# Optimization experiments

Hardware: AMD Instinct MI355X
Metric: run time of the kernel (lower is better)

## Reference

```python
import jax, jax.numpy as jnp
import numpy as np

LEN_M = 131328   # (data_dim+1) * d_h = 513 * 256
D_H = 256
N_MC = 64
DATA_DIM_P1 = 513
N = 4096


def setup_inputs() -> dict:
    key = jax.random.key(0)
    k1, k2, k3, k4 = jax.random.split(key, 4)
    params = jax.random.normal(k1, (2 * LEN_M,), dtype=jnp.float32)
    W1 = jax.random.normal(k2, (D_H + 1,), dtype=jnp.float32)
    x = jax.random.normal(k3, (N, DATA_DIM_P1), dtype=jnp.float32)
    eps = jax.random.normal(k4, (N_MC,), dtype=jnp.float32)
    return {"params": params, "W1": W1, "x": x, "eps": eps}


def reference(params, W1, x, eps):
    # split variational params into means and (relu'd) variances
    m_w0 = params[:LEN_M]                                  # [len_m]
    v_w0 = jax.nn.relu(params[LEN_M:]) + 1e-6              # [len_m]
    # reparameterized MC sampling; NOTE: torch code draws ONE scalar eps per
    # MC sample (randn(m_w0[0].shape) is scalar), shared across all weights.
    samps_w0 = m_w0[:, None] + eps[None, :] * jnp.sqrt(v_w0)[:, None]  # [len_m, M]
    W0 = samps_w0.reshape(DATA_DIM_P1, D_H, N_MC)          # [d+1, h, M]
    # fused batched GEMM replacing the d_h * num_MC_samps tiny matmuls
    x_w0 = jnp.einsum('nd,dhm->nhm', x, W0)                # [N, h, M]
    z = jax.nn.relu(x_w0)
    ones = jnp.ones((x.shape[0], 1, N_MC), dtype=x.dtype)
    z = jnp.concatenate([ones, z], axis=1)                 # [N, h+1, M]
    pred_samps = jnp.einsum('nhm,h->nm', z, W1)            # [N, M]
    return pred_samps, m_w0, v_w0
```

## Files before the change

kernel.cpp:

```cpp
#include <hip/hip_runtime.h>
#include <hip/hip_bf16.h>
#include <math.h>

#define LEN_M   131328
#define D_H     256
#define N_MC    64
#define D_P1    513
#define NROW    4096
#define KPAD    512
#define PRED_ELEMS (NROW * N_MC)

#define XB_ELEMS   (NROW * KPAD)
#define WCBT_ELEMS (512 * 512)

typedef __attribute__((ext_vector_type(8))) short short8;
typedef __attribute__((ext_vector_type(4))) float floatx4;

__global__ __launch_bounds__(256) void prep_kernel(
    const float* __restrict__ params, const float* __restrict__ x,
    float* __restrict__ out, __hip_bfloat16* __restrict__ xb,
    float* __restrict__ wcl, __hip_bfloat16* __restrict__ wcbt)
{
    __shared__ unsigned short T[64][65];
    const int bid = blockIdx.x;
    const int t   = threadIdx.x;

    if (bid < 8192) {
        int i = bid * 256 + t;
        int row = i >> 9, col = i & 511;
        xb[i] = __float2bfloat16(x[row * D_P1 + col]);
        if (i < PRED_ELEMS) out[i] = 0.0f;
        if (i < LEN_M) {
            float m = params[i];
            float v = fmaxf(params[LEN_M + i], 0.0f) + 1e-6f;
            out[PRED_ELEMS + i]         = m;
            out[PRED_ELEMS + LEN_M + i] = v;
            if (i >= 131072) {
                int h = i - 131072;
                wcl[h]       = m;
                wcl[256 + h] = sqrtf(v);
            }
        }
        return;
    }

    const int b2 = bid - 8192;
    const int k0 = (b2 & 7) * 64;
    const int c0 = (b2 >> 3) * 64;
    const int hh = t & 63, kb = t >> 6;
    const bool spart = (c0 >= 256);
    const int hbase = c0 & 255;
    const float* src = params + (spart ? LEN_M : 0);

    #pragma unroll 4
    for (int p = 0; p < 16; ++p) {
        int kk = p * 4 + kb;
        float v = src[(k0 + kk) * 256 + hbase + hh];
        if (spart) v = sqrtf(fmaxf(v, 0.0f) + 1e-6f);
        __hip_bfloat16 b = __float2bfloat16(v);
        T[kk][hh] = *(unsigned short*)&b;
    }
    __syncthreads();

    const int cc = t >> 2, kq = t & 3;
    short8 lo, hi;
    #pragma unroll
    for (int j = 0; j < 8; ++j) lo[j] = (short)T[kq * 16 + j][cc];
    #pragma unroll
    for (int j = 0; j < 8; ++j) hi[j] = (short)T[kq * 16 + 8 + j][cc];
    short* dst = (short*)wcbt + (c0 + cc) * 512 + k0 + kq * 16;
    *(short8*)dst       = lo;
    *(short8*)(dst + 8) = hi;
}

__global__ __launch_bounds__(256) void main_kernel(
    const __hip_bfloat16* __restrict__ xb, const __hip_bfloat16* __restrict__ wcbt,
    const float* __restrict__ wcl, const float* __restrict__ x,
    const float* __restrict__ W1, const float* __restrict__ eps,
    float* __restrict__ out)
{
    __shared__ float Clds[128 * 20];

    const int t = threadIdx.x;
    const int w = t >> 6, lane = t & 63;
    const int lane15 = lane & 15, quad = lane >> 4;
    const int H  = blockIdx.x;
    const int bm = blockIdx.y * 16;

    const int part  = w >> 1;
    const int sub   = (w & 1) * 32;
    const int lcol0 = part * 64 + sub;
    const int gc0   = part * 256 + H * 64 + sub + lane15;

    const float e = eps[lane];
    const int r0 = quad * 4;
    float xl[4];
    #pragma unroll
    for (int r = 0; r < 4; ++r) xl[r] = x[(bm + r0 + r) * D_P1 + 512];

    const short* ap  = (const short*)xb   + (bm + lane15) * 512 + quad * 8;
    const short* bp0 = (const short*)wcbt + (gc0 +  0) * 512 + quad * 8;
    const short* bp1 = (const short*)wcbt + (gc0 + 16) * 512 + quad * 8;

    floatx4 acc0 = {0.f,0.f,0.f,0.f}, acc1 = acc0;

    #pragma unroll 4
    for (int k0 = 0; k0 < 512; k0 += 32) {
        short8 a  = *(const short8*)(ap  + k0);
        short8 b0 = *(const short8*)(bp0 + k0);
        short8 b1 = *(const short8*)(bp1 + k0);
        acc0 = __builtin_amdgcn_mfma_f32_16x16x32_bf16(a, b0, acc0, 0, 0, 0);
        acc1 = __builtin_amdgcn_mfma_f32_16x16x32_bf16(a, b1, acc1, 0, 0, 0);
    }

    floatx4 accs[2] = {acc0, acc1};
    #pragma unroll
    for (int s = 0; s < 2; ++s) {
        const float wl = wcl[gc0 + s * 16];
        float4 vv;
        vv.x = accs[s][0] + xl[0] * wl;
        vv.y = accs[s][1] + xl[1] * wl;
        vv.z = accs[s][2] + xl[2] * wl;
        vv.w = accs[s][3] + xl[3] * wl;
        const int lcol = lcol0 + s * 16 + lane15;
        *(float4*)&Clds[lcol * 20 + r0] = vv;
    }
    __syncthreads();

    const int rb = w * 4;
    const float init = (H == 0) ? W1[0] : 0.0f;
    float accp[4] = {init, init, init, init};

    #pragma unroll 8
    for (int hl = 0; hl < 64; ++hl) {
        const float w1h = W1[1 + H * 64 + hl];
        const float4 a0 = *(const float4*)&Clds[hl * 20 + rb];
        const float4 b0 = *(const float4*)&Clds[(64 + hl) * 20 + rb];
        accp[0] = fmaf(fmaxf(fmaf(e, b0.x, a0.x), 0.f), w1h, accp[0]);
        accp[1] = fmaf(fmaxf(fmaf(e, b0.y, a0.y), 0.f), w1h, accp[1]);
        accp[2] = fmaf(fmaxf(fmaf(e, b0.z, a0.z), 0.f), w1h, accp[2]);
        accp[3] = fmaf(fmaxf(fmaf(e, b0.w, a0.w), 0.f), w1h, accp[3]);
    }

    float* op = out + (bm + rb) * 64 + lane;
    #pragma unroll
    for (int r = 0; r < 4; ++r)
        unsafeAtomicAdd(op + r * 64, accp[r]);
}

extern "C" void kernel_launch(void* const* d_in, const int* in_sizes, int n_in,
                              void* d_out, int out_size, void* d_ws, size_t ws_size,
                              hipStream_t stream)
{
    const float* params = (const float*)d_in[0];
    const float* W1     = (const float*)d_in[1];
    const float* x      = (const float*)d_in[2];
    const float* eps    = (const float*)d_in[3];
    float* out = (float*)d_out;

    __hip_bfloat16* xb   = (__hip_bfloat16*)d_ws;
    __hip_bfloat16* wcbt = xb + XB_ELEMS;
    float*          wcl  = (float*)(wcbt + WCBT_ELEMS);

    prep_kernel<<<8192 + 64, 256, 0, stream>>>(params, x, out, xb, wcl, wcbt);
    main_kernel<<<dim3(4, 256), 256, 0, stream>>>(xb, wcbt, wcl, x, W1, eps, out);
}
```

Before: 99.98 us.

## Stage GEMM tiles in LDS via direct loads and replace atomics with partial-sum reduce

The main kernel now processes 32 rows per block and stages A and B tiles into LDS with global_load_lds, so each loaded tile is shared across waves instead of every wave reading its own operands from global memory. Each wave computes four 16x16 MFMA outputs. The per-H results are written to a partial buffer rather than atomically added to the output, and a new reduce kernel sums the four partials and adds the bias. This also removes the zeroing of the output in the prep kernel. The cost is an extra kernel launch, more partial-buffer memory traffic, and two block-wide barriers per k-step that leave no overlap between loads and compute.

```diff
diff --git a/kernel.cpp b/kernel.cpp
--- a/kernel.cpp
+++ b/kernel.cpp
@@ -16,6 +16,13 @@
 typedef __attribute__((ext_vector_type(8))) short short8;
 typedef __attribute__((ext_vector_type(4))) float floatx4;
 
+__device__ __forceinline__ void gl_lds16(const void* g, void* l)
+{
+    __builtin_amdgcn_global_load_lds(
+        (const __attribute__((address_space(1))) unsigned int*)g,
+        (__attribute__((address_space(3))) unsigned int*)l, 16, 0, 0);
+}
+
 __global__ __launch_bounds__(256) void prep_kernel(
     const float* __restrict__ params, const float* __restrict__ x,
     float* __restrict__ out, __hip_bfloat16* __restrict__ xb,
@@ -29,7 +36,6 @@
         int i = bid * 256 + t;
         int row = i >> 9, col = i & 511;
         xb[i] = __float2bfloat16(x[row * D_P1 + col]);
-        if (i < PRED_ELEMS) out[i] = 0.0f;
         if (i < LEN_M) {
             float m = params[i];
             float v = fmaxf(params[LEN_M + i], 0.0f) + 1e-6f;
@@ -77,75 +83,124 @@
     const __hip_bfloat16* __restrict__ xb, const __hip_bfloat16* __restrict__ wcbt,
     const float* __restrict__ wcl, const float* __restrict__ x,
     const float* __restrict__ W1, const float* __restrict__ eps,
-    float* __restrict__ out)
-{
-    __shared__ float Clds[128 * 20];
+    float* __restrict__ partial)
+{
+    __shared__ char smem[128 * 36 * 4];
+    short* AsS  = (short*)smem;
+    short* BsS  = (short*)(smem + 2048);
+    float* Clds = (float*)smem;
 
     const int t = threadIdx.x;
     const int w = t >> 6, lane = t & 63;
     const int lane15 = lane & 15, quad = lane >> 4;
     const int H  = blockIdx.x;
-    const int bm = blockIdx.y * 16;
-
+    const int bm = blockIdx.y * 32;
+
+    const int rhalf = (w & 1) * 16;
+    const int chalf = (w >> 1) * 64;
     const int part  = w >> 1;
-    const int sub   = (w & 1) * 32;
-    const int lcol0 = part * 64 + sub;
-    const int gc0   = part * 256 + H * 64 + sub + lane15;
+
+    const short* xbs = (const short*)xb;
+    const short* wbs = (const short*)wcbt;
+
+    const short* a_src = xbs + (bm + (t >> 2)) * 512 + (t & 3) * 8;
+    void* a_dst = AsS + t * 8;
+    const int lc0 = t >> 2,        kq0 = t & 3;
+    const int lc1 = (256 + t) >> 2, kq1 = t & 3;
+    const short* b_src0 = wbs + (((lc0 >> 6) * 256) + H * 64 + (lc0 & 63)) * 512 + kq0 * 8;
+    const short* b_src1 = wbs + (((lc1 >> 6) * 256) + H * 64 + (lc1 & 63)) * 512 + kq1 * 8;
+    void* b_dst0 = BsS + t * 8;
+    void* b_dst1 = BsS + (256 + t) * 8;
 
     const float e = eps[lane];
-    const int r0 = quad * 4;
-    float xl[4];
-    #pragma unroll
-    for (int r = 0; r < 4; ++r) xl[r] = x[(bm + r0 + r) * D_P1 + 512];
-
-    const short* ap  = (const short*)xb   + (bm + lane15) * 512 + quad * 8;
-    const short* bp0 = (const short*)wcbt + (gc0 +  0) * 512 + quad * 8;
-    const short* bp1 = (const short*)wcbt + (gc0 + 16) * 512 + quad * 8;
-
-    floatx4 acc0 = {0.f,0.f,0.f,0.f}, acc1 = acc0;
-
-    #pragma unroll 4
-    for (int k0 = 0; k0 < 512; k0 += 32) {
-        short8 a  = *(const short8*)(ap  + k0);
-        short8 b0 = *(const short8*)(bp0 + k0);
-        short8 b1 = *(const short8*)(bp1 + k0);
+    float xl[4], wlv[4];
+    #pragma unroll
+    for (int r = 0; r < 4; ++r)
+        xl[r] = x[(bm + rhalf + quad * 4 + r) * D_P1 + 512];
+    #pragma unroll
+    for (int s = 0; s < 4; ++s)
+        wlv[s] = wcl[part * 256 + H * 64 + s * 16 + lane15];
+
+    floatx4 acc0 = {0.f,0.f,0.f,0.f}, acc1 = acc0, acc2 = acc0, acc3 = acc0;
+
+    const short* a_rd  = AsS + (rhalf + lane15) * 32 + quad * 8;
+    const short* b_rd  = BsS + (chalf + lane15) * 32 + quad * 8;
+
+    for (int ks = 0; ks < 16; ++ks) {
+        const int k0 = ks * 32;
+        if (t < 128) gl_lds16(a_src + k0, a_dst);
+        gl_lds16(b_src0 + k0, b_dst0);
+        gl_lds16(b_src1 + k0, b_dst1);
+        __syncthreads();
+
+        short8 a  = *(const short8*)a_rd;
+        short8 b0 = *(const short8*)(b_rd);
+        short8 b1 = *(const short8*)(b_rd + 16 * 32);
+        short8 b2 = *(const short8*)(b_rd + 32 * 32);
+        short8 b3 = *(const short8*)(b_rd + 48 * 32);
         acc0 = __builtin_amdgcn_mfma_f32_16x16x32_bf16(a, b0, acc0, 0, 0, 0);
         acc1 = __builtin_amdgcn_mfma_f32_16x16x32_bf16(a, b1, acc1, 0, 0, 0);
-    }
-
-    floatx4 accs[2] = {acc0, acc1};
-    #pragma unroll
-    for (int s = 0; s < 2; ++s) {
-        const float wl = wcl[gc0 + s * 16];
+        acc2 = __builtin_amdgcn_mfma_f32_16x16x32_bf16(a, b2, acc2, 0, 0, 0);
+        acc3 = __builtin_amdgcn_mfma_f32_16x16x32_bf16(a, b3, acc3, 0, 0, 0);
+        __syncthreads();
+    }
+
+    floatx4 accs[4] = {acc0, acc1, acc2, acc3};
+    const int r0 = rhalf + quad * 4;
+    #pragma unroll
+    for (int s = 0; s < 4; ++s) {
         float4 vv;
-        vv.x = accs[s][0] + xl[0] * wl;
-        vv.y = accs[s][1] + xl[1] * wl;
-        vv.z = accs[s][2] + xl[2] * wl;
-        vv.w = accs[s][3] + xl[3] * wl;
-        const int lcol = lcol0 + s * 16 + lane15;
-        *(float4*)&Clds[lcol * 20 + r0] = vv;
+        vv.x = accs[s][0] + xl[0] * wlv[s];
+        vv.y = accs[s][1] + xl[1] * wlv[s];
+        vv.z = accs[s][2] + xl[2] * wlv[s];
+        vv.w = accs[s][3] + xl[3] * wlv[s];
+        const int lcol = chalf + s * 16 + lane15;
+        *(float4*)&Clds[lcol * 36 + r0] = vv;
     }
     __syncthreads();
 
-    const int rb = w * 4;
-    const float init = (H == 0) ? W1[0] : 0.0f;
-    float accp[4] = {init, init, init, init};
+    const int rb = w * 8;
+    float accp[8] = {0.f,0.f,0.f,0.f,0.f,0.f,0.f,0.f};
 
     #pragma unroll 8
     for (int hl = 0; hl < 64; ++hl) {
         const float w1h = W1[1 + H * 64 + hl];
-        const float4 a0 = *(const float4*)&Clds[hl * 20 + rb];
-        const float4 b0 = *(const float4*)&Clds[(64 + hl) * 20 + rb];
+        const float4 a0 = *(const float4*)&Clds[hl * 36 + rb];
+        const float4 a1 = *(const float4*)&Clds[hl * 36 + rb + 4];
+        const float4 b0 = *(const float4*)&Clds[(64 + hl) * 36 + rb];
+        const float4 b1 = *(const float4*)&Clds[(64 + hl) * 36 + rb + 4];
         accp[0] = fmaf(fmaxf(fmaf(e, b0.x, a0.x), 0.f), w1h, accp[0]);
         accp[1] = fmaf(fmaxf(fmaf(e, b0.y, a0.y), 0.f), w1h, accp[1]);
         accp[2] = fmaf(fmaxf(fmaf(e, b0.z, a0.z), 0.f), w1h, accp[2]);
         accp[3] = fmaf(fmaxf(fmaf(e, b0.w, a0.w), 0.f), w1h, accp[3]);
-    }
-
-    float* op = out + (bm + rb) * 64 + lane;
-    #pragma unroll
-    for (int r = 0; r < 4; ++r)
-        unsafeAtomicAdd(op + r * 64, accp[r]);
+        accp[4] = fmaf(fmaxf(fmaf(e, b1.x, a1.x), 0.f), w1h, accp[4]);
+        accp[5] = fmaf(fmaxf(fmaf(e, b1.y, a1.y), 0.f), w1h, accp[5]);
+        accp[6] = fmaf(fmaxf(fmaf(e, b1.z, a1.z), 0.f), w1h, accp[6]);
+        accp[7] = fmaf(fmaxf(fmaf(e, b1.w, a1.w), 0.f), w1h, accp[7]);
+    }
+
+    float* op = partial + (H * NROW + bm + rb) * 64 + lane;
+    #pragma unroll
+    for (int r = 0; r < 8; ++r)
+        op[r * 64] = accp[r];
+}
+
+__global__ __launch_bounds__(256) void reduce_kernel(
+    const float* __restrict__ partial, const float* __restrict__ W1,
+    float* __restrict__ out)
+{
+    const int i = (blockIdx.x * 256 + threadIdx.x) * 4;
+    const float4 p0 = *(const float4*)(partial + i);
+    const float4 p1 = *(const float4*)(partial + PRED_ELEMS + i);
+    const float4 p2 = *(const float4*)(partial + 2 * PRED_ELEMS + i);
+    const float4 p3 = *(const float4*)(partial + 3 * PRED_ELEMS + i);
+    const float b = W1[0];
+    float4 o;
+    o.x = b + ((p0.x + p1.x) + (p2.x + p3.x));
+    o.y = b + ((p0.y + p1.y) + (p2.y + p3.y));
+    o.z = b + ((p0.z + p1.z) + (p2.z + p3.z));
+    o.w = b + ((p0.w + p1.w) + (p2.w + p3.w));
+    *(float4*)(out + i) = o;
 }
 
 extern "C" void kernel_launch(void* const* d_in, const int* in_sizes, int n_in,
@@ -161,7 +216,9 @@
     __hip_bfloat16* xb   = (__hip_bfloat16*)d_ws;
     __hip_bfloat16* wcbt = xb + XB_ELEMS;
     float*          wcl  = (float*)(wcbt + WCBT_ELEMS);
+    float*          part = wcl + 512;
 
     prep_kernel<<<8192 + 64, 256, 0, stream>>>(params, x, out, xb, wcl, wcbt);
-    main_kernel<<<dim3(4, 256), 256, 0, stream>>>(xb, wcbt, wcl, x, W1, eps, out);
-}
+    main_kernel<<<dim3(4, 128), 256, 0, stream>>>(xb, wcbt, wcl, x, W1, eps, part);
+    reduce_kernel<<<PRED_ELEMS / 1024, 256, 0, stream>>>(part, W1, out);
+}
```

Result: faster. 89.74 us (-10.2%).

## Fuse x bf16 conversion into main GEMM with LDS staging and larger row tiles

Applied to the files above, without the earlier changes.

Drops the separate pass that converts x to a padded bf16 buffer; the main kernel now reads fp32 x directly, converts it and stores it into swizzled LDS, while W tiles are streamed into LDS through global_load_lds. The row tile per block doubles to 32 with a 2x2 MFMA layout, so each B fragment is reused across two row halves. The epilogue uses packed two-wide FMA, and the last-row bias weights are computed inline instead of coming from a workspace array. This removes the large xb write and read traffic and shrinks the prep grid, at the cost of two block-wide syncs per k-step with no double buffering.

```diff
diff --git a/kernel.cpp b/kernel.cpp
--- a/kernel.cpp
+++ b/kernel.cpp
@@ -3,48 +3,48 @@
 #include <math.h>
 
 #define LEN_M   131328
-#define D_H     256
-#define N_MC    64
 #define D_P1    513
 #define NROW    4096
-#define KPAD    512
-#define PRED_ELEMS (NROW * N_MC)
-
-#define XB_ELEMS   (NROW * KPAD)
-#define WCBT_ELEMS (512 * 512)
+#define PRED_ELEMS (NROW * 64)
 
 typedef __attribute__((ext_vector_type(8))) short short8;
 typedef __attribute__((ext_vector_type(4))) float floatx4;
+typedef __attribute__((ext_vector_type(2))) float v2f;
+
+__device__ __forceinline__ void gl_lds16(const void* g, void* l)
+{
+    __builtin_amdgcn_global_load_lds(
+        (const __attribute__((address_space(1))) unsigned int*)g,
+        (__attribute__((address_space(3))) unsigned int*)l, 16, 0, 0);
+}
+
+__device__ __forceinline__ unsigned short bf16b(float f)
+{
+    __hip_bfloat16 h = __float2bfloat16(f);
+    return *(unsigned short*)&h;
+}
 
 __global__ __launch_bounds__(256) void prep_kernel(
-    const float* __restrict__ params, const float* __restrict__ x,
-    float* __restrict__ out, __hip_bfloat16* __restrict__ xb,
-    float* __restrict__ wcl, __hip_bfloat16* __restrict__ wcbt)
+    const float* __restrict__ params, float* __restrict__ out,
+    __hip_bfloat16* __restrict__ wcbt)
 {
     __shared__ unsigned short T[64][65];
     const int bid = blockIdx.x;
     const int t   = threadIdx.x;
 
-    if (bid < 8192) {
+    if (bid < 1024) {
         int i = bid * 256 + t;
-        int row = i >> 9, col = i & 511;
-        xb[i] = __float2bfloat16(x[row * D_P1 + col]);
-        if (i < PRED_ELEMS) out[i] = 0.0f;
+        out[i] = 0.0f;
         if (i < LEN_M) {
             float m = params[i];
             float v = fmaxf(params[LEN_M + i], 0.0f) + 1e-6f;
             out[PRED_ELEMS + i]         = m;
             out[PRED_ELEMS + LEN_M + i] = v;
-            if (i >= 131072) {
-                int h = i - 131072;
-                wcl[h]       = m;
-                wcl[256 + h] = sqrtf(v);
-            }
         }
         return;
     }
 
-    const int b2 = bid - 8192;
+    const int b2 = bid - 1024;
     const int k0 = (b2 & 7) * 64;
     const int c0 = (b2 >> 3) * 64;
     const int hh = t & 63, kb = t >> 6;
@@ -57,8 +57,7 @@
         int kk = p * 4 + kb;
         float v = src[(k0 + kk) * 256 + hbase + hh];
         if (spart) v = sqrtf(fmaxf(v, 0.0f) + 1e-6f);
-        __hip_bfloat16 b = __float2bfloat16(v);
-        T[kk][hh] = *(unsigned short*)&b;
+        T[kk][hh] = bf16b(v);
     }
     __syncthreads();
 
@@ -68,84 +67,149 @@
     for (int j = 0; j < 8; ++j) lo[j] = (short)T[kq * 16 + j][cc];
     #pragma unroll
     for (int j = 0; j < 8; ++j) hi[j] = (short)T[kq * 16 + 8 + j][cc];
-    short* dst = (short*)wcbt + (c0 + cc) * 512 + k0 + kq * 16;
-    *(short8*)dst       = lo;
-    *(short8*)(dst + 8) = hi;
+
+    const int cR  = c0 + cc;
+    const int swz = (cR >> 1) & 3;
+    const int g1  = (k0 >> 3) + 2 * kq;
+    const int g2  = g1 + 1;
+    const int d1  = cR * 64 + (g1 & ~3) + ((g1 & 3) ^ swz);
+    const int d2  = cR * 64 + (g2 & ~3) + ((g2 & 3) ^ swz);
+    short* wb = (short*)wcbt;
+    *(short8*)(wb + d1 * 8) = lo;
+    *(short8*)(wb + d2 * 8) = hi;
 }
 
 __global__ __launch_bounds__(256) void main_kernel(
-    const __hip_bfloat16* __restrict__ xb, const __hip_bfloat16* __restrict__ wcbt,
-    const float* __restrict__ wcl, const float* __restrict__ x,
-    const float* __restrict__ W1, const float* __restrict__ eps,
-    float* __restrict__ out)
-{
-    __shared__ float Clds[128 * 20];
+    const __hip_bfloat16* __restrict__ wcbt, const float* __restrict__ params,
+    const float* __restrict__ x, const float* __restrict__ W1,
+    const float* __restrict__ eps, float* __restrict__ out)
+{
+    __shared__ char smem[128 * 36 * 4];
+    short* Bs   = (short*)smem;
+    short* As   = (short*)(smem + 8192);
+    float* Clds = (float*)smem;
 
     const int t = threadIdx.x;
-    const int w = t >> 6, lane = t & 63;
+    const int w4 = t >> 6, lane = t & 63;
     const int lane15 = lane & 15, quad = lane >> 4;
     const int H  = blockIdx.x;
-    const int bm = blockIdx.y * 16;
-
-    const int part  = w >> 1;
-    const int sub   = (w & 1) * 32;
-    const int lcol0 = part * 64 + sub;
-    const int gc0   = part * 256 + H * 64 + sub + lane15;
+    const int bm = blockIdx.y * 32;
+
+    const short* wb = (const short*)wcbt;
+    const short* bsrc0; const short* bsrc1; short* bdst0; short* bdst1;
+    {
+        int ch0 = t, ch1 = 256 + t;
+        int lc0 = ch0 >> 2, qs0 = ch0 & 3;
+        int lc1 = ch1 >> 2, qs1 = ch1 & 3;
+        int c0g = H * 64 + lc0 + ((lc0 >> 6) * 192);
+        int c1g = H * 64 + lc1 + ((lc1 >> 6) * 192);
+        bsrc0 = wb + (c0g * 64 + qs0) * 8;
+        bsrc1 = wb + (c1g * 64 + qs1) * 8;
+        bdst0 = Bs + ch0 * 8;
+        bdst1 = Bs + ch1 * 8;
+    }
+
+    const int ar = t >> 3, asub = t & 7;
+    const int aq = asub >> 1, ahalf = asub & 1;
+    const float* axp = x + (bm + ar) * D_P1 + asub * 4;
+    unsigned short* adst = (unsigned short*)As + ar * 32
+                         + ((aq ^ ((ar >> 1) & 3)) * 8) + ahalf * 4;
 
     const float e = eps[lane];
-    const int r0 = quad * 4;
-    float xl[4];
-    #pragma unroll
-    for (int r = 0; r < 4; ++r) xl[r] = x[(bm + r0 + r) * D_P1 + 512];
-
-    const short* ap  = (const short*)xb   + (bm + lane15) * 512 + quad * 8;
-    const short* bp0 = (const short*)wcbt + (gc0 +  0) * 512 + quad * 8;
-    const short* bp1 = (const short*)wcbt + (gc0 + 16) * 512 + quad * 8;
-
-    floatx4 acc0 = {0.f,0.f,0.f,0.f}, acc1 = acc0;
+    float xl[2][4];
+    #pragma unroll
+    for (int rh = 0; rh < 2; ++rh)
+        #pragma unroll
+        for (int i = 0; i < 4; ++i)
+            xl[rh][i] = x[(bm + rh * 16 + quad * 4 + i) * D_P1 + 512];
+    float wl[2];
+    #pragma unroll
+    for (int s = 0; s < 2; ++s) {
+        int lc = w4 * 32 + s * 16 + lane15;
+        int c  = H * 64 + lc + ((lc >> 6) * 192);
+        wl[s] = (c < 256) ? params[131072 + c]
+                          : sqrtf(fmaxf(params[LEN_M + 131072 + (c - 256)], 0.0f) + 1e-6f);
+    }
+
+    const short* afp[2]; const short* bfp[2];
+    #pragma unroll
+    for (int rh = 0; rh < 2; ++rh) {
+        int row = rh * 16 + lane15;
+        afp[rh] = As + row * 32 + ((quad ^ ((row >> 1) & 3)) * 8);
+    }
+    #pragma unroll
+    for (int s = 0; s < 2; ++s) {
+        int lc = w4 * 32 + s * 16 + lane15;
+        bfp[s] = Bs + lc * 32 + ((quad ^ ((lc >> 1) & 3)) * 8);
+    }
+
+    floatx4 acc00 = {0.f,0.f,0.f,0.f}, acc01 = acc00, acc10 = acc00, acc11 = acc00;
+
+    for (int ks = 0; ks < 16; ++ks) {
+        gl_lds16(bsrc0 + ks * 32, bdst0);
+        gl_lds16(bsrc1 + ks * 32, bdst1);
+        float f0 = axp[ks * 32 + 0], f1 = axp[ks * 32 + 1];
+        float f2 = axp[ks * 32 + 2], f3 = axp[ks * 32 + 3];
+        ushort4 pk;
+        pk.x = bf16b(f0); pk.y = bf16b(f1); pk.z = bf16b(f2); pk.w = bf16b(f3);
+        *(ushort4*)adst = pk;
+        __syncthreads();
+
+        short8 a0 = *(const short8*)afp[0];
+        short8 a1 = *(const short8*)afp[1];
+        short8 b0 = *(const short8*)bfp[0];
+        short8 b1 = *(const short8*)bfp[1];
+        acc00 = __builtin_amdgcn_mfma_f32_16x16x32_bf16(a0, b0, acc00, 0, 0, 0);
+        acc01 = __builtin_amdgcn_mfma_f32_16x16x32_bf16(a0, b1, acc01, 0, 0, 0);
+        acc10 = __builtin_amdgcn_mfma_f32_16x16x32_bf16(a1, b0, acc10, 0, 0, 0);
+        acc11 = __builtin_amdgcn_mfma_f32_16x16x32_bf16(a1, b1, acc11, 0, 0, 0);
+        __syncthreads();
+    }
+
+    floatx4 accs[2][2] = {{acc00, acc01}, {acc10, acc11}};
+    #pragma unroll
+    for (int rh = 0; rh < 2; ++rh)
+        #pragma unroll
+        for (int s = 0; s < 2; ++s) {
+            float4 o;
+            o.x = accs[rh][s][0] + xl[rh][0] * wl[s];
+            o.y = accs[rh][s][1] + xl[rh][1] * wl[s];
+            o.z = accs[rh][s][2] + xl[rh][2] * wl[s];
+            o.w = accs[rh][s][3] + xl[rh][3] * wl[s];
+            int lc = w4 * 32 + s * 16 + lane15;
+            int r0 = rh * 16 + quad * 4;
+            *(float4*)&Clds[lc * 36 + r0] = o;
+        }
+    __syncthreads();
+
+    const int rb = w4 * 8;
+    const float binit = (H == 0) ? W1[0] : 0.0f;
+    v2f accp[4];
+    #pragma unroll
+    for (int j = 0; j < 4; ++j) accp[j] = (v2f){binit, binit};
+    const v2f e2 = {e, e};
+    const v2f z2 = {0.f, 0.f};
 
     #pragma unroll 4
-    for (int k0 = 0; k0 < 512; k0 += 32) {
-        short8 a  = *(const short8*)(ap  + k0);
-        short8 b0 = *(const short8*)(bp0 + k0);
-        short8 b1 = *(const short8*)(bp1 + k0);
-        acc0 = __builtin_amdgcn_mfma_f32_16x16x32_bf16(a, b0, acc0, 0, 0, 0);
-        acc1 = __builtin_amdgcn_mfma_f32_16x16x32_bf16(a, b1, acc1, 0, 0, 0);
-    }
-
-    floatx4 accs[2] = {acc0, acc1};
-    #pragma unroll
-    for (int s = 0; s < 2; ++s) {
-        const float wl = wcl[gc0 + s * 16];
-        float4 vv;
-        vv.x = accs[s][0] + xl[0] * wl;
-        vv.y = accs[s][1] + xl[1] * wl;
-        vv.z = accs[s][2] + xl[2] * wl;
-        vv.w = accs[s][3] + xl[3] * wl;
-        const int lcol = lcol0 + s * 16 + lane15;
-        *(float4*)&Clds[lcol * 20 + r0] = vv;
-    }
-    __syncthreads();
-
-    const int rb = w * 4;
-    const float init = (H == 0) ? W1[0] : 0.0f;
-    float accp[4] = {init, init, init, init};
-
-    #pragma unroll 8
-    for (int hl = 0; hl < 64; ++hl) {
-        const float w1h = W1[1 + H * 64 + hl];
-        const float4 a0 = *(const float4*)&Clds[hl * 20 + rb];
-        const float4 b0 = *(const float4*)&Clds[(64 + hl) * 20 + rb];
-        accp[0] = fmaf(fmaxf(fmaf(e, b0.x, a0.x), 0.f), w1h, accp[0]);
-        accp[1] = fmaf(fmaxf(fmaf(e, b0.y, a0.y), 0.f), w1h, accp[1]);
-        accp[2] = fmaf(fmaxf(fmaf(e, b0.z, a0.z), 0.f), w1h, accp[2]);
-        accp[3] = fmaf(fmaxf(fmaf(e, b0.w, a0.w), 0.f), w1h, accp[3]);
+    for (int lh = 0; lh < 64; ++lh) {
+        const float w1h = W1[1 + H * 64 + lh];
+        const v2f w2 = {w1h, w1h};
+        const v2f* ap = (const v2f*)&Clds[lh * 36 + rb];
+        const v2f* bp = (const v2f*)&Clds[(64 + lh) * 36 + rb];
+        #pragma unroll
+        for (int j = 0; j < 4; ++j) {
+            v2f t2 = __builtin_elementwise_fma(e2, bp[j], ap[j]);
+            t2 = __builtin_elementwise_max(t2, z2);
+            accp[j] = __builtin_elementwise_fma(t2, w2, accp[j]);
+        }
     }
 
     float* op = out + (bm + rb) * 64 + lane;
     #pragma unroll
-    for (int r = 0; r < 4; ++r)
-        unsafeAtomicAdd(op + r * 64, accp[r]);
+    for (int j = 0; j < 4; ++j) {
+        unsafeAtomicAdd(op + (2 * j) * 64,     accp[j].x);
+        unsafeAtomicAdd(op + (2 * j + 1) * 64, accp[j].y);
+    }
 }
 
 extern "C" void kernel_launch(void* const* d_in, const int* in_sizes, int n_in,
@@ -157,11 +221,8 @@
     const float* x      = (const float*)d_in[2];
     const float* eps    = (const float*)d_in[3];
     float* out = (float*)d_out;
-
-    __hip_bfloat16* xb   = (__hip_bfloat16*)d_ws;
-    __hip_bfloat16* wcbt = xb + XB_ELEMS;
-    float*          wcl  = (float*)(wcbt + WCBT_ELEMS);
-
-    prep_kernel<<<8192 + 64, 256, 0, stream>>>(params, x, out, xb, wcl, wcbt);
-    main_kernel<<<dim3(4, 256), 256, 0, stream>>>(xb, wcbt, wcl, x, W1, eps, out);
-}
+    __hip_bfloat16* wcbt = (__hip_bfloat16*)d_ws;
+
+    prep_kernel<<<1024 + 64, 256, 0, stream>>>(params, out, wcbt);
+    main_kernel<<<dim3(4, 128), 256, 0, stream>>>(wcbt, params, x, W1, eps, out);
+}
```

New measurement: 85.21 us. 14.8% less time.
